# Kernel optimization log

Hardware: AMD Instinct MI355X
Metric: run time of the kernel (lower is better)

The kernel has to match this reference:

```python
import jax, jax.numpy as jnp
import numpy as np
from jax import lax

B, L, F = 32, 2048, 76   # batch, seq_len, feat_dim
H = 128                  # conv hidden channels
D = 128                  # prototype dim (last 1x1 conv)
P = 128                  # number of prototypes
CLASS_SIZE = 2


def setup_inputs() -> dict:
    key = jax.random.key(0)
    ks = jax.random.split(key, 8)
    w = lambda k, shape: jax.random.normal(k, shape, jnp.float32) * 0.05
    return {
        "x": jax.random.normal(ks[0], (B, L, F), jnp.float32),
        "W1": w(ks[1], (H, F, 5)), "b1": jnp.zeros((H,), jnp.float32),
        "W2": w(ks[2], (H, H, 5)), "b2": jnp.zeros((H,), jnp.float32),
        "W3": w(ks[3], (H, H, 5)), "b3": jnp.zeros((H,), jnp.float32),
        "Wo1": w(ks[4], (D, H)), "bo1": jnp.zeros((D,), jnp.float32),
        "Wo2": w(ks[5], (D, D)), "bo2": jnp.zeros((D,), jnp.float32),
        "prototypes": jax.random.uniform(ks[6], (P, D), jnp.float32),
        "protop_classes": jnp.concatenate([jnp.zeros(P // 2, jnp.int32), jnp.ones(P // 2, jnp.int32)]),
    }


def _conv1d_same(h, W, b):
    # h: (B, C, L), W: (O, C, K=5), symmetric padding 2 == torch padding=k//2
    y = lax.conv_general_dilated(h, W, window_strides=(1,), padding=[(2, 2)],
                                 dimension_numbers=("NCW", "OIW", "NCW"))
    return y + b[None, :, None]


def _maxpool2(h):
    return lax.reduce_window(h, -jnp.inf, lax.max, (1, 1, 2), (1, 1, 2), "VALID")


def reference(x, W1, b1, W2, b2, W3, b3, Wo1, bo1, Wo2, bo2, prototypes, protop_classes):
    h = jnp.transpose(x, (0, 2, 1))  # (B, F, L)
    for W, b in ((W1, b1), (W2, b2), (W3, b3)):
        h = _maxpool2(jax.nn.relu(_conv1d_same(h, W, b)))
    # 1x1 convs as channel matmuls
    h = jax.nn.relu(jnp.einsum("bcl,oc->bol", h, Wo1) + bo1[None, :, None])
    h = jax.nn.relu(jnp.einsum("bcl,oc->bol", h, Wo2) + bo2[None, :, None])
    f = jnp.transpose(h, (0, 2, 1))  # (B, Lp=256, D)
    # l2_conv via ||a-b||^2 = ||a||^2 - 2 a.b + ||b||^2 (same math, GEMM form)
    d2 = (jnp.sum(f * f, axis=-1, keepdims=True)
          - 2.0 * jnp.einsum("bld,pd->blp", f, prototypes)
          + jnp.sum(prototypes * prototypes, axis=-1))  # (B, Lp, P)
    dis = jnp.sqrt(jnp.maximum(d2, 1e-12))
    min_dis = jnp.min(dis, axis=1)  # (B, P): min over patches
    # dis2sim, 'log' activation
    sim = jnp.log((min_dis + 1.0) / (min_dis + 1e-4))
    # init_weights: last_layer.weight[i,j] = 1 if protop_classes[j]==i else -0.5
    lw = jnp.where(protop_classes[None, :] == jnp.arange(CLASS_SIZE)[:, None], 1.0, -0.5)
    out = jax.nn.sigmoid(sim @ lw.T)  # (B, CLASS_SIZE)
    return out, min_dis
```

## Files before the change

### kernel.cpp

```cpp
#include <hip/hip_runtime.h>
#include <cmath>


typedef __attribute__((ext_vector_type(8))) short short8;
typedef __attribute__((ext_vector_type(4))) float f32x4;

__device__ __forceinline__ unsigned short f2bf(float v) {
    union { float f; unsigned u; } x; x.f = v;
    unsigned r = x.u + 0x7fffu + ((x.u >> 16) & 1u);
    return (unsigned short)(r >> 16);
}
__device__ __forceinline__ float bf2f(unsigned short b) {
    union { unsigned u; float f; } x; x.u = ((unsigned)b) << 16;
    return x.f;
}

__device__ void pack_conv_w(int t, int total, const float* __restrict__ W, int C,
                            unsigned short* __restrict__ dst)
{
    if (t >= total) return;
    int lane = t & 63, rest = t >> 6;
    int mf = rest & 7; rest >>= 3;
    int kk = rest % 5, cc = rest / 5;
    int m = mf * 16 + (lane & 15);
    int cb = cc * 32 + (lane >> 4) * 8;
    unsigned short v[8];
#pragma unroll
    for (int j = 0; j < 8; ++j) {
        int c = cb + j;
        v[j] = (c < C) ? f2bf(W[((size_t)m * C + c) * 5 + kk]) : (unsigned short)0;
    }
    *(uint4*)&dst[(size_t)t * 8] = *(uint4*)v;
}

__device__ void pack_mat(int t, const float* __restrict__ M, unsigned short* __restrict__ dst)
{
    if (t >= 2048) return;
    int lane = t & 63, mf = (t >> 6) & 7, cc = t >> 9;
    int m = mf * 16 + (lane & 15);
    int c0 = cc * 32 + (lane >> 4) * 8;
    unsigned short v[8];
#pragma unroll
    for (int j = 0; j < 8; ++j) v[j] = f2bf(M[(size_t)m * 128 + c0 + j]);
    *(uint4*)&dst[(size_t)t * 8] = *(uint4*)v;
}

__global__ __launch_bounds__(256)
void prep_weights_kernel(const float* __restrict__ W1, const float* __restrict__ W2,
                         const float* __restrict__ W3, const float* __restrict__ Wo1,
                         const float* __restrict__ Wo2, const float* __restrict__ protos,
                         unsigned short* A1, unsigned short* A2, unsigned short* A3,
                         unsigned short* AW1, unsigned short* AW2, unsigned short* AP,
                         float* pn, unsigned* pm_bits)
{
    int t = blockIdx.x * 256 + threadIdx.x;
    switch (blockIdx.y) {
    case 0: pack_conv_w(t, 7680,  W1, 76,  A1); break;
    case 1: pack_conv_w(t, 10240, W2, 128, A2); break;
    case 2: pack_conv_w(t, 10240, W3, 128, A3); break;
    case 3: pack_mat(t, Wo1, AW1); break;
    case 4: pack_mat(t, Wo2, AW2); break;
    case 5: pack_mat(t, protos, AP); break;
    case 6:
        if (t < 128) {
            float s = 0.f;
            for (int d = 0; d < 128; ++d) {
                float v = bf2f(f2bf(protos[(size_t)t * 128 + d]));
                s = fmaf(v, v, s);
            }
            pn[t] = s;
        }
        break;
    case 7:
        if (t < 4096) pm_bits[t] = 0x7F800000u;
        break;
    }
}

template <int MF, int NJ, int NCC, int STRIDE, int ROWMAX>
__device__ __forceinline__ void conv_k(const unsigned short* __restrict__ Af,
                                       const unsigned short* __restrict__ sIn,
                                       int nbase, int mf0, int lane,
                                       f32x4 (&acc)[MF][NJ])
{
    const int lc = lane & 15;
    const int lk = (lane >> 4) * 8;
#pragma unroll
    for (int i = 0; i < MF; ++i)
#pragma unroll
        for (int j = 0; j < NJ; ++j) acc[i][j] = (f32x4){0.f, 0.f, 0.f, 0.f};

    for (int cc = 0; cc < NCC; ++cc) {
#pragma unroll
        for (int kk = 0; kk < 5; ++kk) {
            const int step = cc * 5 + kk;
            short8 a[MF];
#pragma unroll
            for (int i = 0; i < MF; ++i)
                a[i] = *(const short8*)&Af[(((size_t)step * 8 + mf0 + i) * 64 + lane) * 8];
            short8 bb[NJ];
#pragma unroll
            for (int j = 0; j < NJ; ++j) {
                int row = nbase + j * 16 + lc + kk;
                if (ROWMAX >= 0) row = min(row, ROWMAX);
                bb[j] = *(const short8*)&sIn[row * STRIDE + cc * 32 + lk];
            }
#pragma unroll
            for (int j = 0; j < NJ; ++j)
#pragma unroll
                for (int i = 0; i < MF; ++i)
                    acc[i][j] = __builtin_amdgcn_mfma_f32_16x16x32_bf16(a[i], bb[j], acc[i][j], 0, 0, 0);
        }
    }
}

__device__ __forceinline__ void gemm_head(const unsigned short* __restrict__ Af,
                                          const unsigned short* __restrict__ s_f,
                                          int mf0h, int lane, f32x4 (&acc)[2])
{
    const int lc = lane & 15;
    const int lk = (lane >> 4) * 8;
    acc[0] = (f32x4){0.f, 0.f, 0.f, 0.f};
    acc[1] = (f32x4){0.f, 0.f, 0.f, 0.f};
#pragma unroll
    for (int cc = 0; cc < 4; ++cc) {
        short8 a[2];
#pragma unroll
        for (int i = 0; i < 2; ++i)
            a[i] = *(const short8*)&Af[(((size_t)cc * 8 + mf0h + i) * 64 + lane) * 8];
        short8 bb = *(const short8*)&s_f[lc * 136 + cc * 32 + lk];
#pragma unroll
        for (int i = 0; i < 2; ++i)
            acc[i] = __builtin_amdgcn_mfma_f32_16x16x32_bf16(a[i], bb, acc[i], 0, 0, 0);
    }
}

__global__ __launch_bounds__(256, 4)
void mega_kernel(const float* __restrict__ x,
                 const unsigned short* __restrict__ A1, const float* __restrict__ b1,
                 const unsigned short* __restrict__ A2, const float* __restrict__ b2,
                 const unsigned short* __restrict__ A3, const float* __restrict__ b3,
                 const unsigned short* __restrict__ AW1, const float* __restrict__ bo1,
                 const unsigned short* __restrict__ AW2, const float* __restrict__ bo2,
                 const unsigned short* __restrict__ AP,  const float* __restrict__ pn,
                 unsigned* __restrict__ pm_bits)
{
    __shared__ __align__(16) unsigned short s_x[100 * 104];
    __shared__ __align__(16) unsigned short s_h1[44 * 136];
    __shared__ float s_cb[768];
    __shared__ float s_part[64];
    __shared__ float s_fn[16];
    unsigned short* s_h2 = s_x;
    unsigned short* s_f  = s_x + 2720;

    const int tid  = threadIdx.x;
    const int u    = blockIdx.x;
    const int b    = blockIdx.y;
    const int lane = tid & 63;
    const int wid  = tid >> 6;
    const int mg   = wid & 1;
    const int ng   = wid >> 1;
    const int mf0  = mg * 4;
    const int lc   = lane & 15;
    const int lq   = (lane >> 4) * 4;

    for (int i = tid; i < 768; i += 256) {
        const float* src = (i < 128) ? b1 : (i < 256) ? b2 : (i < 384) ? b3
                         : (i < 512) ? bo1 : (i < 640) ? bo2 : pn;
        s_cb[i] = src[i & 127];
    }

    const int xbase = 64 * u - 14;
    for (int idx = tid; idx < 100 * 24; idx += 256) {
        int pos = idx / 24, c0 = (idx % 24) * 4;
        int l = xbase + pos;
        unsigned short v[4] = {0, 0, 0, 0};
        if (c0 < 76 && l >= 0 && l < 2048) {
            float4 xv = *(const float4*)&x[((size_t)b * 2048 + l) * 76 + c0];
            v[0] = f2bf(xv.x); v[1] = f2bf(xv.y); v[2] = f2bf(xv.z); v[3] = f2bf(xv.w);
        }
        *(uint2*)&s_x[pos * 104 + c0] = *(uint2*)v;
    }
    __syncthreads();

    {
        f32x4 acc[4][3];
        conv_k<4, 3, 3, 104, -1>(A1, s_x, ng * 48, mf0, lane, acc);

#pragma unroll
        for (int i = 0; i < 4; ++i) {
            const int ch0 = (mf0 + i) * 16 + lq;
#pragma unroll
            for (int j = 0; j < 3; ++j) {
                const int nl = ng * 48 + j * 16 + lc;
                unsigned short pk[4];
#pragma unroll
                for (int r = 0; r < 4; ++r) {
                    float v = fmaxf(acc[i][j][r] + s_cb[ch0 + r], 0.f);
                    float o = __shfl_xor(v, 1);
                    pk[r] = f2bf(fmaxf(v, o));
                }
                if ((lc & 1) == 0) {
                    int rr = nl >> 1;
                    int jg = 32 * u - 6 + rr;
                    if (rr < 44) {
                        uint2 val = (jg >= 0 && jg < 1024) ? *(uint2*)pk : make_uint2(0u, 0u);
                        *(uint2*)&s_h1[rr * 136 + ch0] = val;
                    }
                }
            }
        }
    }
    __syncthreads();

    {
        if (tid < 136) ((uint4*)(s_f + 8 * 136))[tid] = make_uint4(0u, 0u, 0u, 0u);

        f32x4 acc[2][3];
        conv_k<2, 3, 4, 136, 43>(A2, s_h1, 0, wid * 2, lane, acc);

#pragma unroll
        for (int i = 0; i < 2; ++i) {
            const int ch0 = (wid * 2 + i) * 16 + lq;
#pragma unroll
            for (int j = 0; j < 3; ++j) {
                const int nl = j * 16 + lc;
                unsigned short pk[4];
#pragma unroll
                for (int r = 0; r < 4; ++r) {
                    float v = fmaxf(acc[i][j][r] + s_cb[128 + ch0 + r], 0.f);
                    float o = __shfl_xor(v, 1);
                    pk[r] = f2bf(fmaxf(v, o));
                }
                if ((lc & 1) == 0) {
                    int rr = nl >> 1;
                    int jg = 16 * u - 2 + rr;
                    if (rr < 20) {
                        uint2 val = (jg >= 0 && jg < 512) ? *(uint2*)pk : make_uint2(0u, 0u);
                        *(uint2*)&s_h2[rr * 136 + ch0] = val;
                    }
                }
            }
        }
    }
    __syncthreads();

    {
        f32x4 acc[2][1];
        conv_k<2, 1, 4, 136, -1>(A3, s_h2, 0, wid * 2, lane, acc);

#pragma unroll
        for (int i = 0; i < 2; ++i) {
            const int ch0 = (wid * 2 + i) * 16 + lq;
            unsigned short pk[4];
#pragma unroll
            for (int r = 0; r < 4; ++r) {
                float v = fmaxf(acc[i][0][r] + s_cb[256 + ch0 + r], 0.f);
                float o = __shfl_xor(v, 1);
                pk[r] = f2bf(fmaxf(v, o));
            }
            if ((lc & 1) == 0)
                *(uint2*)&s_f[(lc >> 1) * 136 + ch0] = *(uint2*)pk;
        }
    }
    __syncthreads();

    const int mf0h = wid * 2;
    f32x4 hacc[2];

    gemm_head(AW1, s_f, mf0h, lane, hacc);
    __syncthreads();
#pragma unroll
    for (int i = 0; i < 2; ++i) {
        const int ch0 = (mf0h + i) * 16 + lq;
        unsigned short pk[4];
#pragma unroll
        for (int r = 0; r < 4; ++r)
            pk[r] = f2bf(fmaxf(hacc[i][r] + s_cb[384 + ch0 + r], 0.f));
        *(uint2*)&s_f[lc * 136 + ch0] = *(uint2*)pk;
    }
    __syncthreads();

    gemm_head(AW2, s_f, mf0h, lane, hacc);
    __syncthreads();
#pragma unroll
    for (int i = 0; i < 2; ++i) {
        const int ch0 = (mf0h + i) * 16 + lq;
        unsigned short pk[4];
#pragma unroll
        for (int r = 0; r < 4; ++r)
            pk[r] = f2bf(fmaxf(hacc[i][r] + s_cb[512 + ch0 + r], 0.f));
        *(uint2*)&s_f[lc * 136 + ch0] = *(uint2*)pk;
    }
    __syncthreads();

    if (tid < 64) {
        int n = tid >> 2, part = tid & 3;
        float s = 0.f;
        for (int c = part * 32; c < part * 32 + 32; ++c) {
            float v = bf2f(s_f[n * 136 + c]);
            s = fmaf(v, v, s);
        }
        s_part[part * 16 + n] = s;
    }
    __syncthreads();
    if (tid < 16)
        s_fn[tid] = s_part[tid] + s_part[16 + tid] + s_part[32 + tid] + s_part[48 + tid];
    __syncthreads();

    gemm_head(AP, s_f, mf0h, lane, hacc);

#pragma unroll
    for (int i = 0; i < 2; ++i) {
#pragma unroll
        for (int r = 0; r < 4; ++r) {
            const int p = (mf0h + i) * 16 + lq + r;
            float d2 = s_fn[lc] + s_cb[640 + p] - 2.f * hacc[i][r];
            float m = sqrtf(fmaxf(d2, 1e-12f));
#pragma unroll
            for (int s = 1; s < 8; s <<= 1)
                m = fminf(m, __shfl_xor(m, s));
            if (lc == 0)
                atomicMin(&pm_bits[(size_t)b * 128 + p], __float_as_uint(m));
        }
    }
}

__global__ __launch_bounds__(128)
void finalize_kernel(const float* __restrict__ pm,
                     const int* __restrict__ classes,
                     float* __restrict__ out)
{
    __shared__ float r0[128], r1[128];
    const int b = blockIdx.x, p = threadIdx.x;
    float m = pm[(size_t)b * 128 + p];
    out[64 + b * 128 + p] = m;

    float sim = logf((m + 1.0f) / (m + 1e-4f));
    int cls = classes[p];
    r0[p] = (cls == 0) ? sim : -0.5f * sim;
    r1[p] = (cls == 1) ? sim : -0.5f * sim;
    __syncthreads();
    for (int s = 64; s > 0; s >>= 1) {
        if (p < s) { r0[p] += r0[p + s]; r1[p] += r1[p + s]; }
        __syncthreads();
    }
    if (p == 0) {
        out[b * 2 + 0] = 1.f / (1.f + expf(-r0[0]));
        out[b * 2 + 1] = 1.f / (1.f + expf(-r1[0]));
    }
}

extern "C" void kernel_launch(void* const* d_in, const int* in_sizes, int n_in,
                              void* d_out, int out_size, void* d_ws, size_t ws_size,
                              hipStream_t stream)
{
    (void)in_sizes; (void)n_in; (void)out_size; (void)ws_size;
    const float* x    = (const float*)d_in[0];
    const float* W1   = (const float*)d_in[1];
    const float* b1   = (const float*)d_in[2];
    const float* W2   = (const float*)d_in[3];
    const float* b2   = (const float*)d_in[4];
    const float* W3   = (const float*)d_in[5];
    const float* b3   = (const float*)d_in[6];
    const float* Wo1  = (const float*)d_in[7];
    const float* bo1  = (const float*)d_in[8];
    const float* Wo2  = (const float*)d_in[9];
    const float* bo2  = (const float*)d_in[10];
    const float* prot = (const float*)d_in[11];
    const int*   cls  = (const int*)d_in[12];
    float* out = (float*)d_out;

    char* ws = (char*)d_ws;
    unsigned short* A1  = (unsigned short*)(ws);
    unsigned short* A2  = (unsigned short*)(ws + 122880);
    unsigned short* A3  = (unsigned short*)(ws + 286720);
    unsigned short* AW1 = (unsigned short*)(ws + 450560);
    unsigned short* AW2 = (unsigned short*)(ws + 483328);
    unsigned short* AP  = (unsigned short*)(ws + 516096);
    float*          pn  = (float*)(ws + 548864);
    unsigned*       pm  = (unsigned*)(ws + 549376);

    prep_weights_kernel<<<dim3(40, 8), 256, 0, stream>>>(W1, W2, W3, Wo1, Wo2, prot,
                                                         A1, A2, A3, AW1, AW2, AP, pn, pm);
    mega_kernel<<<dim3(32, 32), 256, 0, stream>>>(x, A1, b1, A2, b2, A3, b3,
                                                  AW1, bo1, AW2, bo2, AP, pn, pm);
    finalize_kernel<<<32, 128, 0, stream>>>((const float*)pm, cls, out);
}
```

Before: 126.5 us.

## Fuse finalize into mega kernel, prefetch conv weights, and trim head barriers

The finalize step moves into the main kernel: a per-batch atomic counter lets the last block for each batch compute sim, the sigmoid and the outputs, so one launch disappears when workspace allows. The conv inner loop now prefetches the next step's weight fragments into registers and raises wave priority around the MFMA bursts. The head GEMMs write into a separate LDS buffer, which removes several barriers, and the feature norm is computed from fp32 values in registers. This adds register pressure from the double-buffered fragments and a serialized tail in the last block, and the norm now uses unrounded values instead of bf16-rounded ones.

```diff
diff --git a/kernel.cpp b/kernel.cpp
--- a/kernel.cpp
+++ b/kernel.cpp
@@ -51,7 +51,7 @@
                          const float* __restrict__ Wo2, const float* __restrict__ protos,
                          unsigned short* A1, unsigned short* A2, unsigned short* A3,
                          unsigned short* AW1, unsigned short* AW2, unsigned short* AP,
-                         float* pn, unsigned* pm_bits)
+                         float* pn, unsigned* pm_bits, unsigned* cnt)
 {
     int t = blockIdx.x * 256 + threadIdx.x;
     switch (blockIdx.y) {
@@ -72,7 +72,8 @@
         }
         break;
     case 7:
-        if (t < 4096) pm_bits[t] = 0x7F800000u;
+        if (t < 4096)                    pm_bits[t] = 0x7F800000u;
+        else if (cnt && t < 4128)        cnt[t - 4096] = 0u;
         break;
     }
 }
@@ -85,37 +86,46 @@
 {
     const int lc = lane & 15;
     const int lk = (lane >> 4) * 8;
+    constexpr int NSTEP = NCC * 5;
 #pragma unroll
     for (int i = 0; i < MF; ++i)
 #pragma unroll
         for (int j = 0; j < NJ; ++j) acc[i][j] = (f32x4){0.f, 0.f, 0.f, 0.f};
 
-    for (int cc = 0; cc < NCC; ++cc) {
-#pragma unroll
-        for (int kk = 0; kk < 5; ++kk) {
-            const int step = cc * 5 + kk;
-            short8 a[MF];
+    short8 a_cur[MF], a_nxt[MF];
+#pragma unroll
+    for (int i = 0; i < MF; ++i)
+        a_cur[i] = *(const short8*)&Af[(((size_t)mf0 + i) * 64 + lane) * 8];
+
+#pragma unroll
+    for (int step = 0; step < NSTEP; ++step) {
+        const int kk = step % 5, cc = step / 5;
+        if (step + 1 < NSTEP) {
 #pragma unroll
             for (int i = 0; i < MF; ++i)
-                a[i] = *(const short8*)&Af[(((size_t)step * 8 + mf0 + i) * 64 + lane) * 8];
-            short8 bb[NJ];
-#pragma unroll
-            for (int j = 0; j < NJ; ++j) {
-                int row = nbase + j * 16 + lc + kk;
-                if (ROWMAX >= 0) row = min(row, ROWMAX);
-                bb[j] = *(const short8*)&sIn[row * STRIDE + cc * 32 + lk];
-            }
-#pragma unroll
-            for (int j = 0; j < NJ; ++j)
-#pragma unroll
-                for (int i = 0; i < MF; ++i)
-                    acc[i][j] = __builtin_amdgcn_mfma_f32_16x16x32_bf16(a[i], bb[j], acc[i][j], 0, 0, 0);
-        }
+                a_nxt[i] = *(const short8*)&Af[(((size_t)(step + 1) * 8 + mf0 + i) * 64 + lane) * 8];
+        }
+        short8 bb[NJ];
+#pragma unroll
+        for (int j = 0; j < NJ; ++j) {
+            int row = nbase + j * 16 + lc + kk;
+            if (ROWMAX >= 0) row = min(row, ROWMAX);
+            bb[j] = *(const short8*)&sIn[row * STRIDE + cc * 32 + lk];
+        }
+        __builtin_amdgcn_s_setprio(1);
+#pragma unroll
+        for (int j = 0; j < NJ; ++j)
+#pragma unroll
+            for (int i = 0; i < MF; ++i)
+                acc[i][j] = __builtin_amdgcn_mfma_f32_16x16x32_bf16(a_cur[i], bb[j], acc[i][j], 0, 0, 0);
+        __builtin_amdgcn_s_setprio(0);
+#pragma unroll
+        for (int i = 0; i < MF; ++i) a_cur[i] = a_nxt[i];
     }
 }
 
 __device__ __forceinline__ void gemm_head(const unsigned short* __restrict__ Af,
-                                          const unsigned short* __restrict__ s_f,
+                                          const unsigned short* __restrict__ s_in,
                                           int mf0h, int lane, f32x4 (&acc)[2])
 {
     const int lc = lane & 15;
@@ -128,10 +138,12 @@
 #pragma unroll
         for (int i = 0; i < 2; ++i)
             a[i] = *(const short8*)&Af[(((size_t)cc * 8 + mf0h + i) * 64 + lane) * 8];
-        short8 bb = *(const short8*)&s_f[lc * 136 + cc * 32 + lk];
+        short8 bb = *(const short8*)&s_in[lc * 136 + cc * 32 + lk];
+        __builtin_amdgcn_s_setprio(1);
 #pragma unroll
         for (int i = 0; i < 2; ++i)
             acc[i] = __builtin_amdgcn_mfma_f32_16x16x32_bf16(a[i], bb, acc[i], 0, 0, 0);
+        __builtin_amdgcn_s_setprio(0);
     }
 }
 
@@ -143,15 +155,17 @@
                  const unsigned short* __restrict__ AW1, const float* __restrict__ bo1,
                  const unsigned short* __restrict__ AW2, const float* __restrict__ bo2,
                  const unsigned short* __restrict__ AP,  const float* __restrict__ pn,
-                 unsigned* __restrict__ pm_bits)
+                 unsigned* __restrict__ pm_bits, unsigned* __restrict__ cnt,
+                 const int* __restrict__ classes, float* __restrict__ out)
 {
     __shared__ __align__(16) unsigned short s_x[100 * 104];
     __shared__ __align__(16) unsigned short s_h1[44 * 136];
     __shared__ float s_cb[768];
     __shared__ float s_part[64];
-    __shared__ float s_fn[16];
+    __shared__ unsigned s_last;
     unsigned short* s_h2 = s_x;
     unsigned short* s_f  = s_x + 2720;
+    unsigned short* s_t1 = s_x + 4896;
 
     const int tid  = threadIdx.x;
     const int u    = blockIdx.x;
@@ -269,7 +283,6 @@
     f32x4 hacc[2];
 
     gemm_head(AW1, s_f, mf0h, lane, hacc);
-    __syncthreads();
 #pragma unroll
     for (int i = 0; i < 2; ++i) {
         const int ch0 = (mf0h + i) * 16 + lq;
@@ -277,45 +290,40 @@
 #pragma unroll
         for (int r = 0; r < 4; ++r)
             pk[r] = f2bf(fmaxf(hacc[i][r] + s_cb[384 + ch0 + r], 0.f));
-        *(uint2*)&s_f[lc * 136 + ch0] = *(uint2*)pk;
-    }
-    __syncthreads();
-
-    gemm_head(AW2, s_f, mf0h, lane, hacc);
-    __syncthreads();
-#pragma unroll
-    for (int i = 0; i < 2; ++i) {
-        const int ch0 = (mf0h + i) * 16 + lq;
-        unsigned short pk[4];
-#pragma unroll
-        for (int r = 0; r < 4; ++r)
-            pk[r] = f2bf(fmaxf(hacc[i][r] + s_cb[512 + ch0 + r], 0.f));
-        *(uint2*)&s_f[lc * 136 + ch0] = *(uint2*)pk;
-    }
-    __syncthreads();
-
-    if (tid < 64) {
-        int n = tid >> 2, part = tid & 3;
-        float s = 0.f;
-        for (int c = part * 32; c < part * 32 + 32; ++c) {
-            float v = bf2f(s_f[n * 136 + c]);
-            s = fmaf(v, v, s);
-        }
-        s_part[part * 16 + n] = s;
-    }
-    __syncthreads();
-    if (tid < 16)
-        s_fn[tid] = s_part[tid] + s_part[16 + tid] + s_part[32 + tid] + s_part[48 + tid];
+        *(uint2*)&s_t1[lc * 136 + ch0] = *(uint2*)pk;
+    }
+    __syncthreads();
+
+    gemm_head(AW2, s_t1, mf0h, lane, hacc);
+    {
+        float fnp = 0.f;
+#pragma unroll
+        for (int i = 0; i < 2; ++i) {
+            const int ch0 = (mf0h + i) * 16 + lq;
+            unsigned short pk[4];
+#pragma unroll
+            for (int r = 0; r < 4; ++r) {
+                float v = fmaxf(hacc[i][r] + s_cb[512 + ch0 + r], 0.f);
+                fnp = fmaf(v, v, fnp);
+                pk[r] = f2bf(v);
+            }
+            *(uint2*)&s_f[lc * 136 + ch0] = *(uint2*)pk;
+        }
+        fnp += __shfl_xor(fnp, 16);
+        fnp += __shfl_xor(fnp, 32);
+        if (lane < 16) s_part[wid * 16 + lc] = fnp;
+    }
     __syncthreads();
 
     gemm_head(AP, s_f, mf0h, lane, hacc);
+    const float fn_l = s_part[lc] + s_part[16 + lc] + s_part[32 + lc] + s_part[48 + lc];
 
 #pragma unroll
     for (int i = 0; i < 2; ++i) {
 #pragma unroll
         for (int r = 0; r < 4; ++r) {
             const int p = (mf0h + i) * 16 + lq + r;
-            float d2 = s_fn[lc] + s_cb[640 + p] - 2.f * hacc[i][r];
+            float d2 = fn_l + s_cb[640 + p] - 2.f * hacc[i][r];
             float m = sqrtf(fmaxf(d2, 1e-12f));
 #pragma unroll
             for (int s = 1; s < 8; s <<= 1)
@@ -324,6 +332,38 @@
                 atomicMin(&pm_bits[(size_t)b * 128 + p], __float_as_uint(m));
         }
     }
+
+    if (cnt) {
+        __syncthreads();
+        if (tid == 0) {
+            __threadfence();
+            s_last = atomicAdd(&cnt[b], 1u);
+        }
+        __syncthreads();
+        if (s_last == 31u) {
+            __threadfence();
+            float* r0 = (float*)s_h1;
+            float* r1 = r0 + 128;
+            if (tid < 128) {
+                unsigned mb = atomicOr(&pm_bits[(size_t)b * 128 + tid], 0u);
+                float m = __uint_as_float(mb);
+                out[64 + b * 128 + tid] = m;
+                float sim = logf((m + 1.0f) / (m + 1e-4f));
+                int c = classes[tid];
+                r0[tid] = (c == 0) ? sim : -0.5f * sim;
+                r1[tid] = (c == 1) ? sim : -0.5f * sim;
+            }
+            __syncthreads();
+            for (int s = 64; s > 0; s >>= 1) {
+                if (tid < s) { r0[tid] += r0[tid + s]; r1[tid] += r1[tid + s]; }
+                __syncthreads();
+            }
+            if (tid == 0) {
+                out[b * 2 + 0] = 1.f / (1.f + expf(-r0[0]));
+                out[b * 2 + 1] = 1.f / (1.f + expf(-r1[0]));
+            }
+        }
+    }
 }
 
 __global__ __launch_bounds__(128)
@@ -355,7 +395,7 @@
                               void* d_out, int out_size, void* d_ws, size_t ws_size,
                               hipStream_t stream)
 {
-    (void)in_sizes; (void)n_in; (void)out_size; (void)ws_size;
+    (void)in_sizes; (void)n_in; (void)out_size;
     const float* x    = (const float*)d_in[0];
     const float* W1   = (const float*)d_in[1];
     const float* b1   = (const float*)d_in[2];
@@ -380,10 +420,14 @@
     unsigned short* AP  = (unsigned short*)(ws + 516096);
     float*          pn  = (float*)(ws + 548864);
     unsigned*       pm  = (unsigned*)(ws + 549376);
+    const bool merged = (ws_size >= 565760u + 128u);
+    unsigned*       cnt = merged ? (unsigned*)(ws + 565760) : nullptr;
 
     prep_weights_kernel<<<dim3(40, 8), 256, 0, stream>>>(W1, W2, W3, Wo1, Wo2, prot,
-                                                         A1, A2, A3, AW1, AW2, AP, pn, pm);
+                                                         A1, A2, A3, AW1, AW2, AP, pn, pm, cnt);
     mega_kernel<<<dim3(32, 32), 256, 0, stream>>>(x, A1, b1, A2, b2, A3, b3,
-                                                  AW1, bo1, AW2, bo2, AP, pn, pm);
-    finalize_kernel<<<32, 128, 0, stream>>>((const float*)pm, cls, out);
-}
+                                                  AW1, bo1, AW2, bo2, AP, pn, pm, cnt,
+                                                  cls, out);
+    if (!merged)
+        finalize_kernel<<<32, 128, 0, stream>>>((const float*)pm, cls, out);
+}
```

Result: slower. 152.6 us (+20.6%).
